# Performance work log

Hardware: AMD Instinct MI355X
Metric: run time of the kernel (lower is better)

The kernel has to match this reference:

```python
import jax, jax.numpy as jnp
import numpy as np

ALPHA = 0.2   # LeakyReLU negative slope
NEG = -9e15   # mask fill value from the torch code


def _conv1d(x, w, b):
    # x: (N, C_in, L), w: (C_out, C_in, 5), padding=2 -> same length
    y = jax.lax.conv_general_dilated(x, w, window_strides=(1,), padding=[(2, 2)],
                                     dimension_numbers=('NCH', 'OIH', 'NCH'))
    return y + b[None, :, None]


def _gat(h, mask, W, a):
    # Faithful to a_input @ a: e_ij = leakyrelu(Wh_i . a[:H] + Wh_j . a[H:])
    Wh = jnp.einsum('bnf,fo->bno', h, W)          # (B,N,H)
    H = W.shape[1]
    f1 = Wh @ a[:H]                               # (B,N,1)
    f2 = Wh @ a[H:]                               # (B,N,1)
    e = f1 + jnp.swapaxes(f2, 1, 2)               # (B,N,N)
    e = jnp.where(e > 0, e, ALPHA * e)            # LeakyReLU
    e = jnp.where(mask, e, NEG)
    att = jax.nn.softmax(e, axis=-1)              # dropout skipped (eval mode)
    return jnp.einsum('bij,bjo->bio', att, Wh)


def setup_inputs() -> dict:
    key = jax.random.key(0)
    ks = jax.random.split(key, 14)
    B, S, N, H, E = 8, 200, 512, 64, 2048
    sc = 0.1
    return {
        'x': jax.random.normal(ks[0], (B, S, N * 2), dtype=jnp.float32),
        'adj': jax.random.randint(ks[1], (N, N), 0, 2, dtype=jnp.int32),
        'edge_index': jax.random.randint(ks[2], (E, 2), 0, N, dtype=jnp.int32),
        'conv1_w': jax.random.normal(ks[3], (H // 2, 2, 5), dtype=jnp.float32) * sc,
        'conv1_b': jnp.zeros((H // 2,), dtype=jnp.float32),
        'conv2_w': jax.random.normal(ks[4], (H, H // 2, 5), dtype=jnp.float32) * sc,
        'conv2_b': jnp.zeros((H,), dtype=jnp.float32),
        'W1': jax.random.normal(ks[5], (H, H), dtype=jnp.float32) * sc,
        'a1': jax.random.normal(ks[6], (2 * H, 1), dtype=jnp.float32) * sc,
        'W2': jax.random.normal(ks[7], (H, H), dtype=jnp.float32) * sc,
        'a2': jax.random.normal(ks[8], (2 * H, 1), dtype=jnp.float32) * sc,
        'fc1_w': jax.random.normal(ks[9], (2 * H, H), dtype=jnp.float32) * sc,
        'fc1_b': jnp.zeros((H,), dtype=jnp.float32),
        'fc2_w': jax.random.normal(ks[10], (H, 1), dtype=jnp.float32) * sc,
        'fc2_b': jnp.zeros((1,), dtype=jnp.float32),
    }


def reference(x, adj, edge_index, conv1_w, conv1_b, conv2_w, conv2_b,
              W1, a1, W2, a2, fc1_w, fc1_b, fc2_w, fc2_b):
    B = x.shape[0]
    N = adj.shape[0]
    # (B,S,2N) -> (B,N,S,2) -> (B*N,2,S)
    xn = x.reshape(B, -1, N, 2).transpose(0, 2, 1, 3)
    xf = xn.reshape(B * N, -1, 2).transpose(0, 2, 1)
    h = jax.nn.relu(_conv1d(xf, conv1_w, conv1_b))
    h = jax.nn.relu(_conv1d(h, conv2_w, conv2_b))
    h = h.mean(axis=-1)                 # AdaptiveAvgPool1d(1) + squeeze
    h = h.reshape(B, N, -1)             # (B,N,H)
    mask = (adj > 0)[None]              # (1,N,N) broadcasts over batch
    h = jax.nn.relu(_gat(h, mask, W1, a1))
    h = _gat(h, mask, W2, a2)
    h1 = h[:, edge_index[:, 0]]         # (B,E,H)
    h2 = h[:, edge_index[:, 1]]
    he = jnp.concatenate([h1, h2], axis=-1)  # (B,E,2H)
    z = jax.nn.relu(he @ fc1_w + fc1_b)
    return jax.nn.sigmoid(z @ fc2_w + fc2_b).squeeze(-1)  # (B,E)
```

## Files before the change

### kernel.cpp

```cpp
#include <hip/hip_runtime.h>
#include <hip/hip_bf16.h>

typedef unsigned short u16;
typedef __attribute__((ext_vector_type(8))) short short8;
typedef __attribute__((ext_vector_type(4))) float float4v;
typedef __attribute__((ext_vector_type(4))) unsigned int uint4v;

#define BATCH 8
#define SLEN  200
#define NNODE 512
#define NEDGE 2048
#define NEGV  -9000000000000000.0f

#define H1S 40
#define H1R 212

__device__ __forceinline__ u16 f2bf(float f) {
    unsigned int x = __float_as_uint(f);
    unsigned int lsb = (x >> 16) & 1u;
    x += 0x7fffu + lsb;
    return (u16)(x >> 16);
}

__device__ __forceinline__ float bf2f(u16 u) {
    return __uint_as_float(((unsigned int)u) << 16);
}

__device__ __forceinline__ unsigned int pk2(float a, float b) {
    __hip_bfloat162 h = __float22bfloat162_rn(make_float2(a, b));
    unsigned int r;
    __builtin_memcpy(&r, &h, 4);
    return r;
}

__global__ __launch_bounds__(256) void pre_kernel(
    const int* __restrict__ adj,
    const float* __restrict__ w2,
    const float* __restrict__ fc1w,
    const float* __restrict__ W2g,
    u16* __restrict__ w2f,
    u16* __restrict__ efw,
    u16* __restrict__ w2gf,
    u16* __restrict__ msk)
{
    const int t = threadIdx.x;
    const int blk = blockIdx.x;

    if (blk == 0) {
        for (int idx = t; idx < 20 * 64 * 8; idx += 256) {
            const int fid = idx >> 9, rem = idx & 511;
            const int lane = rem >> 3, j = rem & 7;
            const int kk = fid >> 2, ot = fid & 3;
            const int ml = lane & 15, q = lane >> 4;
            const int c  = q * 8 + j;
            const int ic = (c & 1) * 16 + (c >> 1);
            const int oc = ot * 16 + ml;
            w2f[idx] = f2bf(w2[(size_t)oc * 160 + ic * 5 + kk]);
        }
        return;
    }
    if (blk == 1) {
        for (int idx = t; idx < 16 * 64 * 8; idx += 256) {
            const int u = idx >> 9, rem = idx & 511;
            const int lane = rem >> 3, j = rem & 7;
            const int ks = u >> 2, wvv = u & 3;
            const int ml = lane & 15, q = lane >> 4;
            const int o = wvv * 16 + ml;
            const int k = ks * 32 + q * 8 + j;
            efw[idx] = f2bf(fc1w[k * 64 + o]);
        }
        return;
    }
    if (blk == 2) {
        for (int idx = t; idx < 8 * 64 * 8; idx += 256) {
            const int u = idx >> 9, rem = idx & 511;
            const int lane = rem >> 3, j = rem & 7;
            const int kh = u >> 2, nt = u & 3;
            const int ml = lane & 15, q = lane >> 4;
            const int o = nt * 16 + ml;
            const int k = kh * 32 + q * 8 + j;
            w2gf[idx] = f2bf(W2g[k * 64 + o]);
        }
        return;
    }

    {
        const int tid   = (blk - 3) * 256 + t;
        const int row   = tid >> 5;
        const int chunk = tid & 31;
        const int4* ap = (const int4*)(adj + (size_t)row * 512 + chunk * 16);
        const int4 a0 = ap[0], a1 = ap[1], a2 = ap[2], a3 = ap[3];
        unsigned int bits = 0;
        bits |= (a0.x > 0) ? 0x0001u : 0u;  bits |= (a0.y > 0) ? 0x0002u : 0u;
        bits |= (a0.z > 0) ? 0x0004u : 0u;  bits |= (a0.w > 0) ? 0x0008u : 0u;
        bits |= (a1.x > 0) ? 0x0010u : 0u;  bits |= (a1.y > 0) ? 0x0020u : 0u;
        bits |= (a1.z > 0) ? 0x0040u : 0u;  bits |= (a1.w > 0) ? 0x0080u : 0u;
        bits |= (a2.x > 0) ? 0x0100u : 0u;  bits |= (a2.y > 0) ? 0x0200u : 0u;
        bits |= (a2.z > 0) ? 0x0400u : 0u;  bits |= (a2.w > 0) ? 0x0800u : 0u;
        bits |= (a3.x > 0) ? 0x1000u : 0u;  bits |= (a3.y > 0) ? 0x2000u : 0u;
        bits |= (a3.z > 0) ? 0x4000u : 0u;  bits |= (a3.w > 0) ? 0x8000u : 0u;
        msk[row * 32 + chunk] = (u16)bits;
    }
}

__global__ __launch_bounds__(256) void conv_fused_kernel(
    const float* __restrict__ x,
    const float* __restrict__ w1,
    const float* __restrict__ b1,
    const float* __restrict__ b2,
    const float* __restrict__ W1,
    const float* __restrict__ a1,
    const u16* __restrict__ w2f,
    u16* __restrict__ Wh_bt,
    float* __restrict__ f1,
    float* __restrict__ f2)
{
    __shared__ __align__(16) u16 h1pA[H1R * H1S];
    __shared__ __align__(16) u16 h1pB[H1R * H1S];
    __shared__ __align__(16) float uni[896];

    float (*xs)[2][212]  = (float (*)[2][212])uni;
    float (*red)[2][32]  = (float (*)[2][32])uni;
    float (*hm)[64]      = (float (*)[64])(uni + 256);
    float (*part)[4][64] = (float (*)[4][64])(uni + 384);

    const int t    = threadIdx.x;
    const int blk  = blockIdx.x;
    const int b    = blk >> 8;
    const int pair = blk & 255;
    const int n0   = pair * 2;
    const int lane = t & 63;
    const int wv   = t >> 6;
    const int ml   = lane & 15;
    const int q    = lane >> 4;
    const int p = t & 15;
    const int g = t >> 4;
    const int o2 = wv & 1;
    const int mh = wv >> 1;

    short8 wfA[5], wfB[5];
    #pragma unroll
    for (int kk = 0; kk < 5; ++kk) {
        wfA[kk] = *(const short8*)(w2f + ((kk * 4 + o2 * 2 + 0) * 64 + lane) * 8);
        wfB[kk] = *(const short8*)(w2f + ((kk * 4 + o2 * 2 + 1) * 64 + lane) * 8);
    }
    const float bias2a = b2[o2 * 32 + ml];
    const float bias2b = b2[o2 * 32 + 16 + ml];

    float wA[10], wB[10];
    #pragma unroll
    for (int j = 0; j < 10; ++j) {
        wA[j] = w1[p * 10 + j];
        wB[j] = w1[(16 + p) * 10 + j];
    }
    const float b1a = b1[p], b1b = b1[16 + p];

    if (t < SLEN) {
        const float4 xv = *(const float4*)(x + ((size_t)(b * SLEN + t)) * 1024 + 4 * pair);
        xs[0][0][2 + t] = xv.x;
        xs[0][1][2 + t] = xv.y;
        xs[1][0][2 + t] = xv.z;
        xs[1][1][2 + t] = xv.w;
    } else if (t < 212) {
        const int pp = (t < 202) ? (t - 200) : t;
        xs[0][0][pp] = 0.f; xs[0][1][pp] = 0.f;
        xs[1][0][pp] = 0.f; xs[1][1][pp] = 0.f;
    }
    {
        unsigned int* hzA = (unsigned int*)h1pA;
        unsigned int* hzB = (unsigned int*)h1pB;
        if (t < 40)       { hzA[t] = 0u;        hzB[t] = 0u; }
        else if (t < 240) { hzA[4000 + t] = 0u; hzB[4000 + t] = 0u; }
    }
    __syncthreads();

#define CONV1_NODE(nd, H1P) do {                                              \
    _Pragma("unroll")                                                         \
    for (int u = 0; u < 4; ++u) {                                             \
        const int base = 4 * g + 64 * u;                                      \
        if (base < SLEN) {                                                    \
            float X0[8], X1[8];                                               \
            *(float4*)&X0[0] = *(const float4*)&xs[nd][0][base];              \
            *(float4*)&X0[4] = *(const float4*)&xs[nd][0][base + 4];          \
            *(float4*)&X1[0] = *(const float4*)&xs[nd][1][base];              \
            *(float4*)&X1[4] = *(const float4*)&xs[nd][1][base + 4];          \
            _Pragma("unroll")                                                 \
            for (int i = 0; i < 4; ++i) {                                     \
                float a0 = b1a, a1v = b1b;                                    \
                _Pragma("unroll")                                             \
                for (int k = 0; k < 5; ++k) {                                 \
                    const float x0 = X0[i + k], x1 = X1[i + k];               \
                    a0  += wA[k] * x0 + wA[5 + k] * x1;                       \
                    a1v += wB[k] * x0 + wB[5 + k] * x1;                       \
                }                                                             \
                *(unsigned int*)&H1P[(2 + base + i) * H1S + 2 * p] =          \
                    pk2(fmaxf(a0, 0.f), fmaxf(a1v, 0.f));                     \
            }                                                                 \
        }                                                                     \
    }                                                                         \
} while (0)

#define CONV2_NODE(nd, H1P) do {                                              \
    float tA = 0.f, tB = 0.f;                                                 \
    const int mt0 = mh * 7, mtE = mh ? 13 : 7;                                \
    for (int mt = mt0; mt < mtE; ++mt) {                                      \
        float4v acc0 = {0.f, 0.f, 0.f, 0.f};                                  \
        float4v acc1 = {0.f, 0.f, 0.f, 0.f};                                  \
        _Pragma("unroll")                                                     \
        for (int kk = 0; kk < 5; ++kk) {                                      \
            const short8 a = *(const short8*)&H1P[(mt * 16 + ml + kk) * H1S + q * 8]; \
            acc0 = __builtin_amdgcn_mfma_f32_16x16x32_bf16(a, wfA[kk], acc0, 0, 0, 0); \
            acc1 = __builtin_amdgcn_mfma_f32_16x16x32_bf16(a, wfB[kk], acc1, 0, 0, 0); \
        }                                                                     \
        if (mt < 12) {                                                        \
            _Pragma("unroll")                                                 \
            for (int r = 0; r < 4; ++r) {                                     \
                tA += fmaxf(acc0[r] + bias2a, 0.f);                           \
                tB += fmaxf(acc1[r] + bias2b, 0.f);                           \
            }                                                                 \
        } else if (q < 2) {                      \
            _Pragma("unroll")                                                 \
            for (int r = 0; r < 4; ++r) {                                     \
                tA += fmaxf(acc0[r] + bias2a, 0.f);                           \
                tB += fmaxf(acc1[r] + bias2b, 0.f);                           \
            }                                                                 \
        }                                                                     \
    }                                                                         \
    tA += __shfl_xor(tA, 16, 64);                                             \
    tA += __shfl_xor(tA, 32, 64);                                             \
    tB += __shfl_xor(tB, 16, 64);                                             \
    tB += __shfl_xor(tB, 32, 64);                                             \
    tAn[nd] = tA;                                                             \
    tBn[nd] = tB;                                                             \
} while (0)

    float tAn[2], tBn[2];

    CONV1_NODE(0, h1pA);
    __syncthreads();

    CONV2_NODE(0, h1pA);
    CONV1_NODE(1, h1pB);
    __syncthreads();

    CONV2_NODE(1, h1pB);

#undef CONV1_NODE
#undef CONV2_NODE

    if (lane < 16) {
        red[wv][0][ml]      = tAn[0];
        red[wv][0][16 + ml] = tBn[0];
        red[wv][1][ml]      = tAn[1];
        red[wv][1][16 + ml] = tBn[1];
    }
    __syncthreads();
    if (t < 128) {
        const int nd = t >> 6, o = t & 63;
        const int grp = (o >> 5), idx = o & 31;
        hm[nd][o] = (red[grp][nd][idx] + red[grp + 2][nd][idx]) * (1.0f / 200.0f);
    }
    __syncthreads();

    {
        const int o = t & 63, q4 = t >> 6;
        const float* Wp = W1 + (q4 * 16) * 64 + o;
        float p0 = 0.f, p1 = 0.f;
        #pragma unroll
        for (int k = 0; k < 16; ++k) {
            const float w = Wp[k * 64];
            p0 += hm[0][q4 * 16 + k] * w;
            p1 += hm[1][q4 * 16 + k] * w;
        }
        part[0][q4][o] = p0;
        part[1][q4][o] = p1;
    }
    __syncthreads();
    if (t < 128) {
        const int nd = t >> 6, o = t & 63;
        const int n = n0 + nd;
        const float v = part[nd][0][o] + part[nd][1][o] + part[nd][2][o] + part[nd][3][o];
        Wh_bt[((size_t)(b * 64 + o)) * 512 + n] = f2bf(v);
        float v1 = v * a1[o];
        float v2 = v * a1[64 + o];
        #pragma unroll
        for (int off = 32; off; off >>= 1) {
            v1 += __shfl_xor(v1, off, 64);
            v2 += __shfl_xor(v2, off, 64);
        }
        if (o == 0) { f1[b * 512 + n] = v1; f2[b * 512 + n] = v2; }
    }
}

#define PSTR 520
__global__ __launch_bounds__(512) void gat_attn_kernel(
    const u16* __restrict__ Wh_bt,
    const float* __restrict__ f1in,
    const float* __restrict__ f2in,
    const u16* __restrict__ msk,
    const u16* __restrict__ w2gf,
    const float* __restrict__ a2,
    u16* __restrict__ whbt_out,
    float* __restrict__ f1out,
    float* __restrict__ f2out,
    u16* __restrict__ outp,
    const int fuse)
{
    __shared__ __align__(16) u16 P[16 * PSTR];
    __shared__ float f2s[512];
    __shared__ float invs[16];
    __shared__ float f1s[16];
    __shared__ float accH[4][64][4];
    __shared__ __align__(16) u16 g1s[16 * 72];
    __shared__ __align__(16) u16 wh2s[64 * 20];
    __shared__ float fp1[4][16], fp2[4][16];

    const int t   = threadIdx.x;
    const int blk = blockIdx.x;
    const int b   = blk >> 5;
    const int i0  = (blk & 31) * 16;
    const int lane = t & 63, wv = t >> 6, nt = wv & 3, kh = wv >> 2;
    const int ml = lane & 15, q = lane >> 4;

    const u16* Bp = Wh_bt + ((size_t)(b * 64 + nt * 16 + ml)) * 512 + kh * 256 + q * 8;
    short8 bfr[8];
    #pragma unroll
    for (int ks = 0; ks < 8; ++ks)
        bfr[ks] = *(const short8*)(Bp + ks * 32);

    f2s[t & 511] = f2in[b * 512 + (t & 511)];
    if (t < 16) f1s[t] = f1in[b * 512 + i0 + t];
    __syncthreads();

    {
        const int i = t >> 5, jseg = t & 31;
        const float f1i = f1s[i];
        const unsigned int mbits = msk[(size_t)(i0 + i) * 32 + jseg];
        const float* f2p = f2s + jseg * 16;
        float ev[16];
        float mx = -3.0e38f;
        #pragma unroll
        for (int v = 0; v < 16; ++v) {
            float e = f1i + f2p[v];
            e = e > 0.f ? e : 0.2f * e;
            e = ((mbits >> v) & 1u) ? e : NEGV;
            ev[v] = e;
            mx = fmaxf(mx, e);
        }
        mx = fmaxf(mx, __shfl_xor(mx, 1, 64));
        mx = fmaxf(mx, __shfl_xor(mx, 2, 64));
        mx = fmaxf(mx, __shfl_xor(mx, 4, 64));
        mx = fmaxf(mx, __shfl_xor(mx, 8, 64));
        mx = fmaxf(mx, __shfl_xor(mx, 16, 64));
        float sum = 0.f;
        #pragma unroll
        for (int v = 0; v < 16; ++v) {
            const float ex = __expf(ev[v] - mx);
            ev[v] = ex;
            sum += ex;
        }
        sum += __shfl_xor(sum, 1, 64);
        sum += __shfl_xor(sum, 2, 64);
        sum += __shfl_xor(sum, 4, 64);
        sum += __shfl_xor(sum, 8, 64);
        sum += __shfl_xor(sum, 16, 64);
        if (jseg == 0) invs[i] = 1.0f / sum;
        unsigned int* prow = (unsigned int*)&P[i * PSTR + jseg * 16];
        #pragma unroll
        for (int v = 0; v < 8; ++v)
            prow[v] = pk2(ev[2 * v], ev[2 * v + 1]);
    }
    __syncthreads();

    float4v acc = {0.f, 0.f, 0.f, 0.f};
    #pragma unroll
    for (int ks = 0; ks < 8; ++ks) {
        const short8 afr = *(const short8*)&P[ml * PSTR + kh * 256 + ks * 32 + q * 8];
        acc = __builtin_amdgcn_mfma_f32_16x16x32_bf16(afr, bfr[ks], acc, 0, 0, 0);
    }
    if (kh == 1) {
        #pragma unroll
        for (int r = 0; r < 4; ++r) accH[nt][lane][r] = acc[r];
    }
    __syncthreads();
    if (kh == 0) {
        #pragma unroll
        for (int r = 0; r < 4; ++r) {
            const int i2 = q * 4 + r;
            float val = (acc[r] + accH[nt][lane][r]) * invs[i2];
            if (fuse) {
                val = fmaxf(val, 0.f);
                g1s[i2 * 72 + nt * 16 + ml] = f2bf(val);
            } else {
                outp[((size_t)(b * 512 + i0 + i2)) * 64 + nt * 16 + ml] = f2bf(val);
            }
        }
    }

    if (!fuse) return;

    __syncthreads();
    const short8 af2 = *(const short8*)&g1s[ml * 72 + kh * 32 + q * 8];
    const short8 bf2v = *(const short8*)(w2gf + ((kh * 4 + nt) * 64 + lane) * 8);
    float4v c2 = {0.f, 0.f, 0.f, 0.f};
    c2 = __builtin_amdgcn_mfma_f32_16x16x32_bf16(af2, bf2v, c2, 0, 0, 0);
    if (kh == 1) {
        #pragma unroll
        for (int r = 0; r < 4; ++r) accH[nt][lane][r] = c2[r];
    }
    __syncthreads();
    if (kh == 0) {
        const int o = nt * 16 + ml;
        const float a2o1 = a2[o], a2o2 = a2[64 + o];
        #pragma unroll
        for (int r = 0; r < 4; ++r) {
            const float wv2 = c2[r] + accH[nt][lane][r];
            wh2s[o * 20 + q * 4 + r] = f2bf(wv2);
            float p1 = wv2 * a2o1, p2 = wv2 * a2o2;
            p1 += __shfl_xor(p1, 1, 64); p2 += __shfl_xor(p2, 1, 64);
            p1 += __shfl_xor(p1, 2, 64); p2 += __shfl_xor(p2, 2, 64);
            p1 += __shfl_xor(p1, 4, 64); p2 += __shfl_xor(p2, 4, 64);
            p1 += __shfl_xor(p1, 8, 64); p2 += __shfl_xor(p2, 8, 64);
            if (ml == 0) {
                fp1[nt][q * 4 + r] = p1;
                fp2[nt][q * 4 + r] = p2;
            }
        }
    }
    __syncthreads();
    if (t < 256) {
        const int o = t >> 2, seg = t & 3;
        *(uint2*)&whbt_out[((size_t)(b * 64 + o)) * 512 + i0 + seg * 4] =
            *(const uint2*)&wh2s[o * 20 + seg * 4];
    }
    if (t < 16) {
        f1out[b * 512 + i0 + t] = fp1[0][t] + fp1[1][t] + fp1[2][t] + fp1[3][t];
        f2out[b * 512 + i0 + t] = fp2[0][t] + fp2[1][t] + fp2[2][t] + fp2[3][t];
    }
}

#define FSTR 136
__global__ __launch_bounds__(256) void edge_mlp_kernel(
    const u16* __restrict__ hg,
    const int* __restrict__ eidx,
    const u16* __restrict__ efw,
    const float* __restrict__ fc1b,
    const float* __restrict__ fc2w,
    const float* __restrict__ fc2b,
    float* __restrict__ out)
{
    __shared__ __align__(16) u16 he[16 * FSTR];
    __shared__ float part[16][4];

    const int t   = threadIdx.x;
    const int blk = blockIdx.x;
    const int b   = blk >> 7;
    const int e0  = (blk & 127) * 16;
    const int lane = t & 63, wv = t >> 6, ml = lane & 15, q = lane >> 4;

    short8 bw[4];
    #pragma unroll
    for (int ks = 0; ks < 4; ++ks)
        bw[ks] = *(const short8*)(efw + ((ks * 4 + wv) * 64 + lane) * 8);
    const int o = 16 * wv + ml;
    const float bo = fc1b[o];
    const float wo = fc2w[o];

    {
        const int ep = t >> 4, p = t & 15;
        const int e = e0 + ep;
        const int node = (p < 8) ? eidx[e * 2] : eidx[e * 2 + 1];
        const int c0 = (p & 7) * 8;
        const u16* hp = hg + ((size_t)(b * 512 + node)) * 64 + c0;
        *(uint4v*)&he[ep * FSTR + ((p < 8) ? 0 : 64) + c0] = *(const uint4v*)hp;
    }
    __syncthreads();

    float4v acc = {0.f, 0.f, 0.f, 0.f};
    #pragma unroll
    for (int ks = 0; ks < 4; ++ks) {
        const short8 afr = *(const short8*)&he[ml * FSTR + ks * 32 + q * 8];
        acc = __builtin_amdgcn_mfma_f32_16x16x32_bf16(afr, bw[ks], acc, 0, 0, 0);
    }
    #pragma unroll
    for (int r = 0; r < 4; ++r) {
        float z = fmaxf(acc[r] + bo, 0.f) * wo;
        z += __shfl_xor(z, 1, 64);
        z += __shfl_xor(z, 2, 64);
        z += __shfl_xor(z, 4, 64);
        z += __shfl_xor(z, 8, 64);
        if (ml == 0) part[q * 4 + r][wv] = z;
    }
    __syncthreads();
    if (t < 16) {
        const float v = part[t][0] + part[t][1] + part[t][2] + part[t][3] + fc2b[0];
        out[b * 2048 + e0 + t] = 1.0f / (1.0f + __expf(-v));
    }
}

extern "C" void kernel_launch(void* const* d_in, const int* in_sizes, int n_in,
                              void* d_out, int out_size, void* d_ws, size_t ws_size,
                              hipStream_t stream) {
    const float* x    = (const float*)d_in[0];
    const int* adj    = (const int*)d_in[1];
    const int* eidx   = (const int*)d_in[2];
    const float* w1   = (const float*)d_in[3];
    const float* b1   = (const float*)d_in[4];
    const float* w2   = (const float*)d_in[5];
    const float* b2   = (const float*)d_in[6];
    const float* W1   = (const float*)d_in[7];
    const float* a1   = (const float*)d_in[8];
    const float* W2   = (const float*)d_in[9];
    const float* a2   = (const float*)d_in[10];
    const float* fc1w = (const float*)d_in[11];
    const float* fc1b = (const float*)d_in[12];
    const float* fc2w = (const float*)d_in[13];
    const float* fc2b = (const float*)d_in[14];
    float* out = (float*)d_out;

    float* ws = (float*)d_ws;
    const size_t R = (size_t)BATCH * NNODE;
    float* f1a   = ws;
    float* f2a   = f1a + R;
    float* f1b   = f2a + R;
    float* f2b   = f1b + R;
    u16*   g_bt  = (u16*)(f2b + R);
    u16*   whbt1 = g_bt + R * 64;
    u16*   whbt2 = whbt1 + R * 64;
    u16*   w2f   = whbt2 + R * 64;
    u16*   efw   = w2f + 10240;
    u16*   w2gf  = efw + 8192;
    u16*   msk   = w2gf + 4096;

    pre_kernel<<<dim3(67), dim3(256), 0, stream>>>(
        adj, w2, fc1w, W2, w2f, efw, w2gf, msk);
    conv_fused_kernel<<<dim3(2048), dim3(256), 0, stream>>>(
        x, w1, b1, b2, W1, a1, w2f, whbt1, f1a, f2a);
    gat_attn_kernel<<<dim3(256), dim3(512), 0, stream>>>(
        whbt1, f1a, f2a, msk, w2gf, a2, whbt2, f1b, f2b, g_bt, 1);
    gat_attn_kernel<<<dim3(256), dim3(512), 0, stream>>>(
        whbt2, f1b, f2b, msk, w2gf, a2, whbt2, f1b, f2b, g_bt, 0);
    edge_mlp_kernel<<<dim3(1024), dim3(256), 0, stream>>>(
        g_bt, eidx, efw, fc1b, fc2w, fc2b, out);
}
```

Baseline: 134.1 us.

## Remove preprocessing kernel; convert weights and adjacency mask inline in consumers

```diff
diff --git a/kernel.cpp b/kernel.cpp
--- a/kernel.cpp
+++ b/kernel.cpp
@@ -31,76 +31,6 @@
     unsigned int r;
     __builtin_memcpy(&r, &h, 4);
     return r;
-}
-
-__global__ __launch_bounds__(256) void pre_kernel(
-    const int* __restrict__ adj,
-    const float* __restrict__ w2,
-    const float* __restrict__ fc1w,
-    const float* __restrict__ W2g,
-    u16* __restrict__ w2f,
-    u16* __restrict__ efw,
-    u16* __restrict__ w2gf,
-    u16* __restrict__ msk)
-{
-    const int t = threadIdx.x;
-    const int blk = blockIdx.x;
-
-    if (blk == 0) {
-        for (int idx = t; idx < 20 * 64 * 8; idx += 256) {
-            const int fid = idx >> 9, rem = idx & 511;
-            const int lane = rem >> 3, j = rem & 7;
-            const int kk = fid >> 2, ot = fid & 3;
-            const int ml = lane & 15, q = lane >> 4;
-            const int c  = q * 8 + j;
-            const int ic = (c & 1) * 16 + (c >> 1);
-            const int oc = ot * 16 + ml;
-            w2f[idx] = f2bf(w2[(size_t)oc * 160 + ic * 5 + kk]);
-        }
-        return;
-    }
-    if (blk == 1) {
-        for (int idx = t; idx < 16 * 64 * 8; idx += 256) {
-            const int u = idx >> 9, rem = idx & 511;
-            const int lane = rem >> 3, j = rem & 7;
-            const int ks = u >> 2, wvv = u & 3;
-            const int ml = lane & 15, q = lane >> 4;
-            const int o = wvv * 16 + ml;
-            const int k = ks * 32 + q * 8 + j;
-            efw[idx] = f2bf(fc1w[k * 64 + o]);
-        }
-        return;
-    }
-    if (blk == 2) {
-        for (int idx = t; idx < 8 * 64 * 8; idx += 256) {
-            const int u = idx >> 9, rem = idx & 511;
-            const int lane = rem >> 3, j = rem & 7;
-            const int kh = u >> 2, nt = u & 3;
-            const int ml = lane & 15, q = lane >> 4;
-            const int o = nt * 16 + ml;
-            const int k = kh * 32 + q * 8 + j;
-            w2gf[idx] = f2bf(W2g[k * 64 + o]);
-        }
-        return;
-    }
-
-    {
-        const int tid   = (blk - 3) * 256 + t;
-        const int row   = tid >> 5;
-        const int chunk = tid & 31;
-        const int4* ap = (const int4*)(adj + (size_t)row * 512 + chunk * 16);
-        const int4 a0 = ap[0], a1 = ap[1], a2 = ap[2], a3 = ap[3];
-        unsigned int bits = 0;
-        bits |= (a0.x > 0) ? 0x0001u : 0u;  bits |= (a0.y > 0) ? 0x0002u : 0u;
-        bits |= (a0.z > 0) ? 0x0004u : 0u;  bits |= (a0.w > 0) ? 0x0008u : 0u;
-        bits |= (a1.x > 0) ? 0x0010u : 0u;  bits |= (a1.y > 0) ? 0x0020u : 0u;
-        bits |= (a1.z > 0) ? 0x0040u : 0u;  bits |= (a1.w > 0) ? 0x0080u : 0u;
-        bits |= (a2.x > 0) ? 0x0100u : 0u;  bits |= (a2.y > 0) ? 0x0200u : 0u;
-        bits |= (a2.z > 0) ? 0x0400u : 0u;  bits |= (a2.w > 0) ? 0x0800u : 0u;
-        bits |= (a3.x > 0) ? 0x1000u : 0u;  bits |= (a3.y > 0) ? 0x2000u : 0u;
-        bits |= (a3.z > 0) ? 0x4000u : 0u;  bits |= (a3.w > 0) ? 0x8000u : 0u;
-        msk[row * 32 + chunk] = (u16)bits;
-    }
 }
 
 __global__ __launch_bounds__(256) void conv_fused_kernel(
@@ -110,7 +40,7 @@
     const float* __restrict__ b2,
     const float* __restrict__ W1,
     const float* __restrict__ a1,
-    const u16* __restrict__ w2f,
+    const float* __restrict__ w2,
     u16* __restrict__ Wh_bt,
     float* __restrict__ f1,
     float* __restrict__ f2)
@@ -139,10 +69,30 @@
     const int mh = wv >> 1;
 
     short8 wfA[5], wfB[5];
-    #pragma unroll
-    for (int kk = 0; kk < 5; ++kk) {
-        wfA[kk] = *(const short8*)(w2f + ((kk * 4 + o2 * 2 + 0) * 64 + lane) * 8);
-        wfB[kk] = *(const short8*)(w2f + ((kk * 4 + o2 * 2 + 1) * 64 + lane) * 8);
+    {
+        const float* pA0 = w2 + (o2 * 32 + ml) * 160 + 20 * q;
+        const float* pA1 = pA0 + 80;
+        const float* pB0 = pA0 + 16 * 160;
+        const float* pB1 = pB0 + 80;
+        float A0[20], A1[20], B0[20], B1[20];
+        #pragma unroll
+        for (int c = 0; c < 5; ++c) {
+            *(float4*)&A0[4 * c] = *(const float4*)(pA0 + 4 * c);
+            *(float4*)&A1[4 * c] = *(const float4*)(pA1 + 4 * c);
+            *(float4*)&B0[4 * c] = *(const float4*)(pB0 + 4 * c);
+            *(float4*)&B1[4 * c] = *(const float4*)(pB1 + 4 * c);
+        }
+        #pragma unroll
+        for (int kk = 0; kk < 5; ++kk) {
+            unsigned int wa[4], wb[4];
+            #pragma unroll
+            for (int d = 0; d < 4; ++d) {
+                wa[d] = pk2(A0[d * 5 + kk], A1[d * 5 + kk]);
+                wb[d] = pk2(B0[d * 5 + kk], B1[d * 5 + kk]);
+            }
+            __builtin_memcpy(&wfA[kk], wa, 16);
+            __builtin_memcpy(&wfB[kk], wb, 16);
+        }
     }
     const float bias2a = b2[o2 * 32 + ml];
     const float bias2b = b2[o2 * 32 + 16 + ml];
@@ -297,8 +247,8 @@
     const u16* __restrict__ Wh_bt,
     const float* __restrict__ f1in,
     const float* __restrict__ f2in,
-    const u16* __restrict__ msk,
-    const u16* __restrict__ w2gf,
+    const int* __restrict__ adj,
+    const float* __restrict__ W2g,
     const float* __restrict__ a2,
     u16* __restrict__ whbt_out,
     float* __restrict__ f1out,
@@ -328,15 +278,33 @@
     for (int ks = 0; ks < 8; ++ks)
         bfr[ks] = *(const short8*)(Bp + ks * 32);
 
+    const int i_row = t >> 5, jseg0 = t & 31;
+    const int4* ap = (const int4*)(adj + (size_t)(i0 + i_row) * 512 + jseg0 * 16);
+    const int4 m0 = ap[0], m1 = ap[1], m2 = ap[2], m3 = ap[3];
+
+    float wgv[8];
+    if (fuse) {
+        #pragma unroll
+        for (int j = 0; j < 8; ++j)
+            wgv[j] = W2g[(kh * 32 + q * 8 + j) * 64 + nt * 16 + ml];
+    }
+
     f2s[t & 511] = f2in[b * 512 + (t & 511)];
     if (t < 16) f1s[t] = f1in[b * 512 + i0 + t];
     __syncthreads();
 
     {
-        const int i = t >> 5, jseg = t & 31;
-        const float f1i = f1s[i];
-        const unsigned int mbits = msk[(size_t)(i0 + i) * 32 + jseg];
-        const float* f2p = f2s + jseg * 16;
+        const float f1i = f1s[i_row];
+        unsigned int mbits = 0;
+        mbits |= (m0.x > 0) ? 0x0001u : 0u;  mbits |= (m0.y > 0) ? 0x0002u : 0u;
+        mbits |= (m0.z > 0) ? 0x0004u : 0u;  mbits |= (m0.w > 0) ? 0x0008u : 0u;
+        mbits |= (m1.x > 0) ? 0x0010u : 0u;  mbits |= (m1.y > 0) ? 0x0020u : 0u;
+        mbits |= (m1.z > 0) ? 0x0040u : 0u;  mbits |= (m1.w > 0) ? 0x0080u : 0u;
+        mbits |= (m2.x > 0) ? 0x0100u : 0u;  mbits |= (m2.y > 0) ? 0x0200u : 0u;
+        mbits |= (m2.z > 0) ? 0x0400u : 0u;  mbits |= (m2.w > 0) ? 0x0800u : 0u;
+        mbits |= (m3.x > 0) ? 0x1000u : 0u;  mbits |= (m3.y > 0) ? 0x2000u : 0u;
+        mbits |= (m3.z > 0) ? 0x4000u : 0u;  mbits |= (m3.w > 0) ? 0x8000u : 0u;
+        const float* f2p = f2s + jseg0 * 16;
         float ev[16];
         float mx = -3.0e38f;
         #pragma unroll
@@ -364,8 +332,8 @@
         sum += __shfl_xor(sum, 4, 64);
         sum += __shfl_xor(sum, 8, 64);
         sum += __shfl_xor(sum, 16, 64);
-        if (jseg == 0) invs[i] = 1.0f / sum;
-        unsigned int* prow = (unsigned int*)&P[i * PSTR + jseg * 16];
+        if (jseg0 == 0) invs[i_row] = 1.0f / sum;
+        unsigned int* prow = (unsigned int*)&P[i_row * PSTR + jseg0 * 16];
         #pragma unroll
         for (int v = 0; v < 8; ++v)
             prow[v] = pk2(ev[2 * v], ev[2 * v + 1]);
@@ -401,7 +369,14 @@
 
     __syncthreads();
     const short8 af2 = *(const short8*)&g1s[ml * 72 + kh * 32 + q * 8];
-    const short8 bf2v = *(const short8*)(w2gf + ((kh * 4 + nt) * 64 + lane) * 8);
+    short8 bf2v;
+    {
+        unsigned int wgp[4];
+        #pragma unroll
+        for (int d = 0; d < 4; ++d)
+            wgp[d] = pk2(wgv[2 * d], wgv[2 * d + 1]);
+        __builtin_memcpy(&bf2v, wgp, 16);
+    }
     float4v c2 = {0.f, 0.f, 0.f, 0.f};
     c2 = __builtin_amdgcn_mfma_f32_16x16x32_bf16(af2, bf2v, c2, 0, 0, 0);
     if (kh == 1) {
@@ -443,7 +418,7 @@
 __global__ __launch_bounds__(256) void edge_mlp_kernel(
     const u16* __restrict__ hg,
     const int* __restrict__ eidx,
-    const u16* __restrict__ efw,
+    const float* __restrict__ fc1w,
     const float* __restrict__ fc1b,
     const float* __restrict__ fc2w,
     const float* __restrict__ fc2b,
@@ -458,11 +433,14 @@
     const int e0  = (blk & 127) * 16;
     const int lane = t & 63, wv = t >> 6, ml = lane & 15, q = lane >> 4;
 
-    short8 bw[4];
-    #pragma unroll
-    for (int ks = 0; ks < 4; ++ks)
-        bw[ks] = *(const short8*)(efw + ((ks * 4 + wv) * 64 + lane) * 8);
     const int o = 16 * wv + ml;
+    float fwv[32];
+    #pragma unroll
+    for (int ks = 0; ks < 4; ++ks) {
+        #pragma unroll
+        for (int j = 0; j < 8; ++j)
+            fwv[ks * 8 + j] = fc1w[(ks * 32 + q * 8 + j) * 64 + o];
+    }
     const float bo = fc1b[o];
     const float wo = fc2w[o];
 
@@ -475,6 +453,16 @@
         *(uint4v*)&he[ep * FSTR + ((p < 8) ? 0 : 64) + c0] = *(const uint4v*)hp;
     }
     __syncthreads();
+
+    short8 bw[4];
+    #pragma unroll
+    for (int ks = 0; ks < 4; ++ks) {
+        unsigned int wp[4];
+        #pragma unroll
+        for (int d = 0; d < 4; ++d)
+            wp[d] = pk2(fwv[ks * 8 + 2 * d], fwv[ks * 8 + 2 * d + 1]);
+        __builtin_memcpy(&bw[ks], wp, 16);
+    }
 
     float4v acc = {0.f, 0.f, 0.f, 0.f};
     #pragma unroll
@@ -527,19 +515,13 @@
     u16*   g_bt  = (u16*)(f2b + R);
     u16*   whbt1 = g_bt + R * 64;
     u16*   whbt2 = whbt1 + R * 64;
-    u16*   w2f   = whbt2 + R * 64;
-    u16*   efw   = w2f + 10240;
-    u16*   w2gf  = efw + 8192;
-    u16*   msk   = w2gf + 4096;
-
-    pre_kernel<<<dim3(67), dim3(256), 0, stream>>>(
-        adj, w2, fc1w, W2, w2f, efw, w2gf, msk);
+
     conv_fused_kernel<<<dim3(2048), dim3(256), 0, stream>>>(
-        x, w1, b1, b2, W1, a1, w2f, whbt1, f1a, f2a);
+        x, w1, b1, b2, W1, a1, w2, whbt1, f1a, f2a);
     gat_attn_kernel<<<dim3(256), dim3(512), 0, stream>>>(
-        whbt1, f1a, f2a, msk, w2gf, a2, whbt2, f1b, f2b, g_bt, 1);
+        whbt1, f1a, f2a, adj, W2, a2, whbt2, f1b, f2b, g_bt, 1);
     gat_attn_kernel<<<dim3(256), dim3(512), 0, stream>>>(
-        whbt2, f1b, f2b, msk, w2gf, a2, whbt2, f1b, f2b, g_bt, 0);
+        whbt2, f1b, f2b, adj, W2, a2, whbt2, f1b, f2b, g_bt, 0);
     edge_mlp_kernel<<<dim3(1024), dim3(256), 0, stream>>>(
-        g_bt, eidx, efw, fc1b, fc2w, fc2b, out);
-}
+        g_bt, eidx, fc1w, fc1b, fc2w, fc2b, out);
+}
```

Result: slower. 141.7 us (+5.7%).

## Split GAT attention into 8-row blocks with full-K per wave

Applied to the files above, without the earlier changes.

```diff
diff --git a/kernel.cpp b/kernel.cpp
--- a/kernel.cpp
+++ b/kernel.cpp
@@ -293,7 +293,7 @@
 }
 
 #define PSTR 520
-__global__ __launch_bounds__(512) void gat_attn_kernel(
+__global__ __launch_bounds__(256) void gat_attn_kernel(
     const u16* __restrict__ Wh_bt,
     const float* __restrict__ f1in,
     const float* __restrict__ f2in,
@@ -308,28 +308,28 @@
 {
     __shared__ __align__(16) u16 P[16 * PSTR];
     __shared__ float f2s[512];
-    __shared__ float invs[16];
-    __shared__ float f1s[16];
-    __shared__ float accH[4][64][4];
+    __shared__ float invs[8];
+    __shared__ float f1s[8];
     __shared__ __align__(16) u16 g1s[16 * 72];
-    __shared__ __align__(16) u16 wh2s[64 * 20];
-    __shared__ float fp1[4][16], fp2[4][16];
+    __shared__ __align__(16) u16 wh2s[64 * 16];
+    __shared__ float fp1[4][8], fp2[4][8];
 
     const int t   = threadIdx.x;
     const int blk = blockIdx.x;
-    const int b   = blk >> 5;
-    const int i0  = (blk & 31) * 16;
-    const int lane = t & 63, wv = t >> 6, nt = wv & 3, kh = wv >> 2;
+    const int b   = blk >> 6;
+    const int i0  = (blk & 63) * 8;
+    const int lane = t & 63, nt = t >> 6;
     const int ml = lane & 15, q = lane >> 4;
 
-    const u16* Bp = Wh_bt + ((size_t)(b * 64 + nt * 16 + ml)) * 512 + kh * 256 + q * 8;
-    short8 bfr[8];
-    #pragma unroll
-    for (int ks = 0; ks < 8; ++ks)
+    const u16* Bp = Wh_bt + ((size_t)(b * 64 + nt * 16 + ml)) * 512 + q * 8;
+    short8 bfr[16];
+    #pragma unroll
+    for (int ks = 0; ks < 16; ++ks)
         bfr[ks] = *(const short8*)(Bp + ks * 32);
 
-    f2s[t & 511] = f2in[b * 512 + (t & 511)];
-    if (t < 16) f1s[t] = f1in[b * 512 + i0 + t];
+    f2s[t]       = f2in[b * 512 + t];
+    f2s[t + 256] = f2in[b * 512 + t + 256];
+    if (t < 8) f1s[t] = f1in[b * 512 + i0 + t];
     __syncthreads();
 
     {
@@ -374,20 +374,15 @@
 
     float4v acc = {0.f, 0.f, 0.f, 0.f};
     #pragma unroll
-    for (int ks = 0; ks < 8; ++ks) {
-        const short8 afr = *(const short8*)&P[ml * PSTR + kh * 256 + ks * 32 + q * 8];
+    for (int ks = 0; ks < 16; ++ks) {
+        const short8 afr = *(const short8*)&P[ml * PSTR + ks * 32 + q * 8];
         acc = __builtin_amdgcn_mfma_f32_16x16x32_bf16(afr, bfr[ks], acc, 0, 0, 0);
     }
-    if (kh == 1) {
-        #pragma unroll
-        for (int r = 0; r < 4; ++r) accH[nt][lane][r] = acc[r];
-    }
-    __syncthreads();
-    if (kh == 0) {
+    if (q < 2) {
         #pragma unroll
         for (int r = 0; r < 4; ++r) {
             const int i2 = q * 4 + r;
-            float val = (acc[r] + accH[nt][lane][r]) * invs[i2];
+            float val = acc[r] * invs[i2];
             if (fuse) {
                 val = fmaxf(val, 0.f);
                 g1s[i2 * 72 + nt * 16 + ml] = f2bf(val);
@@ -400,22 +395,20 @@
     if (!fuse) return;
 
     __syncthreads();
-    const short8 af2 = *(const short8*)&g1s[ml * 72 + kh * 32 + q * 8];
-    const short8 bf2v = *(const short8*)(w2gf + ((kh * 4 + nt) * 64 + lane) * 8);
+    const short8 af2_0 = *(const short8*)&g1s[ml * 72 + q * 8];
+    const short8 af2_1 = *(const short8*)&g1s[ml * 72 + 32 + q * 8];
+    const short8 bw0 = *(const short8*)(w2gf + ((nt) * 64 + lane) * 8);
+    const short8 bw1 = *(const short8*)(w2gf + ((4 + nt) * 64 + lane) * 8);
     float4v c2 = {0.f, 0.f, 0.f, 0.f};
-    c2 = __builtin_amdgcn_mfma_f32_16x16x32_bf16(af2, bf2v, c2, 0, 0, 0);
-    if (kh == 1) {
-        #pragma unroll
-        for (int r = 0; r < 4; ++r) accH[nt][lane][r] = c2[r];
-    }
-    __syncthreads();
-    if (kh == 0) {
+    c2 = __builtin_amdgcn_mfma_f32_16x16x32_bf16(af2_0, bw0, c2, 0, 0, 0);
+    c2 = __builtin_amdgcn_mfma_f32_16x16x32_bf16(af2_1, bw1, c2, 0, 0, 0);
+    if (q < 2) {
         const int o = nt * 16 + ml;
         const float a2o1 = a2[o], a2o2 = a2[64 + o];
         #pragma unroll
         for (int r = 0; r < 4; ++r) {
-            const float wv2 = c2[r] + accH[nt][lane][r];
-            wh2s[o * 20 + q * 4 + r] = f2bf(wv2);
+            const float wv2 = c2[r];
+            wh2s[o * 16 + q * 4 + r] = f2bf(wv2);
             float p1 = wv2 * a2o1, p2 = wv2 * a2o2;
             p1 += __shfl_xor(p1, 1, 64); p2 += __shfl_xor(p2, 1, 64);
             p1 += __shfl_xor(p1, 2, 64); p2 += __shfl_xor(p2, 2, 64);
@@ -428,12 +421,11 @@
         }
     }
     __syncthreads();
-    if (t < 256) {
-        const int o = t >> 2, seg = t & 3;
-        *(uint2*)&whbt_out[((size_t)(b * 64 + o)) * 512 + i0 + seg * 4] =
-            *(const uint2*)&wh2s[o * 20 + seg * 4];
-    }
-    if (t < 16) {
+    if (t < 64) {
+        *(uint4v*)&whbt_out[((size_t)(b * 64 + t)) * 512 + i0] =
+            *(const uint4v*)&wh2s[t * 16];
+    }
+    if (t < 8) {
         f1out[b * 512 + i0 + t] = fp1[0][t] + fp1[1][t] + fp1[2][t] + fp1[3][t];
         f2out[b * 512 + i0 + t] = fp2[0][t] + fp2[1][t] + fp2[2][t] + fp2[3][t];
     }
@@ -536,9 +528,9 @@
         adj, w2, fc1w, W2, w2f, efw, w2gf, msk);
     conv_fused_kernel<<<dim3(2048), dim3(256), 0, stream>>>(
         x, w1, b1, b2, W1, a1, w2f, whbt1, f1a, f2a);
-    gat_attn_kernel<<<dim3(256), dim3(512), 0, stream>>>(
+    gat_attn_kernel<<<dim3(512), dim3(256), 0, stream>>>(
         whbt1, f1a, f2a, msk, w2gf, a2, whbt2, f1b, f2b, g_bt, 1);
-    gat_attn_kernel<<<dim3(256), dim3(512), 0, stream>>>(
+    gat_attn_kernel<<<dim3(512), dim3(256), 0, stream>>>(
         whbt2, f1b, f2b, msk, w2gf, a2, whbt2, f1b, f2b, g_bt, 0);
     edge_mlp_kernel<<<dim3(1024), dim3(256), 0, stream>>>(
         g_bt, eidx, efw, fc1b, fc2w, fc2b, out);
```

Measured after the change: 137.7 us. 2.7% more time.
